# Kernel optimization log

Measured on AMD Instinct MI355X. Metric: run time of the kernel, lower is better.

## Reference

```python
import jax, jax.numpy as jnp
import numpy as np

KEEP_RATIO = 0.25
BLOCK = 8
TEMP = 0.1


def setup_inputs() -> dict:
    key = jax.random.key(0)
    features = jax.random.normal(key, (8, 256, 132, 132), dtype=jnp.float32)
    return {"features": features, "enabled": 1}


def reference(features, enabled):
    B, C, H, W = features.shape
    if not enabled:
        return jnp.ones((B, C, H, W), dtype=features.dtype)
    # pad H, W up to multiples of BLOCK (zeros, like F.pad default)
    ph = (-H) % BLOCK
    pw = (-W) % BLOCK
    x = jnp.pad(jnp.abs(features), ((0, 0), (0, 0), (0, ph), (0, pw)))
    Hp, Wp = H + ph, W + pw
    nh, nw = Hp // BLOCK, Wp // BLOCK
    # avg_pool2d(kernel=stride=BLOCK) == block-mean via reshape
    pooled = x.reshape(B, C, nh, BLOCK, nw, BLOCK).mean(axis=(3, 5))  # [B,C,nh,nw]
    total = nh * nw
    scores = pooled.reshape(B, C, total)
    keep = max(1, min(total, int(round(total * KEEP_RATIO))))
    top_vals, top_idx = jax.lax.top_k(scores, keep)  # sorted descending, like torch.topk
    # hard mask: scatter ones at topk indices
    flat_idx = top_idx.reshape(B * C, keep)
    hard = (jnp.zeros((B * C, total), dtype=features.dtype)
            .at[jnp.arange(B * C)[:, None], flat_idx].set(1.0)
            .reshape(B, C, total))
    # training-mode straight-through soft blend
    thr = jax.lax.stop_gradient(top_vals[..., -1:])  # kth value as threshold
    soft = jax.nn.sigmoid((scores - thr) / TEMP)
    soft = soft * (keep / jnp.maximum(soft.sum(-1, keepdims=True), 1e-6))
    soft = jnp.clip(soft, 0.0, 1.0)
    mask = jax.lax.stop_gradient(hard) - jax.lax.stop_gradient(soft) + soft
    # upsample blocks back to pixels (repeat_interleave) and crop padding
    block_mask = mask.reshape(B, C, nh, nw)
    full = jnp.repeat(jnp.repeat(block_mask, BLOCK, axis=2), BLOCK, axis=3)
    return full[:, :, :H, :W]
```

## Files before the change

### kernel.cpp

```cpp
#include <hip/hip_runtime.h>


#define HH 132
#define WW 132
#define NB 17
#define TOTAL 289
#define KEEP 72
#define NTHREADS 256
#define NV ((HH * WW) / 4)

typedef float floatx4 __attribute__((ext_vector_type(4)));

__global__ __launch_bounds__(NTHREADS)
void gate_kernel(const float4* __restrict__ feats4,
                 const int* __restrict__ enabled_p,
                 float4* __restrict__ out4) {
    const int plane = blockIdx.x;
    const int t = threadIdx.x;
    const float4* __restrict__ fp = feats4 + (size_t)plane * NV;
    floatx4* __restrict__ op = (floatx4*)(out4 + (size_t)plane * NV);

    __shared__ __align__(16) double s_score[TOTAL + 1];
    __shared__ float s_hard[TOTAL];

    for (int i = t; i < TOTAL + 1; i += NTHREADS)
        s_score[i] = (i < TOTAL) ? 0.0 : -1.0e300;
    __syncthreads();

    for (int v = t; v < NV; v += NTHREADS) {
        const float4 x = fp[v];
        const double s = (double)fabsf(x.x) + (double)fabsf(x.y)
                       + (double)fabsf(x.z) + (double)fabsf(x.w);
        const int base = v * 4;
        const int row = base / WW;
        const int col = base - row * WW;
        atomicAdd(&s_score[(row >> 3) * NB + (col >> 3)], s);
    }
    __syncthreads();

    const int en = *enabled_p;
    const double2* __restrict__ sc2 = (const double2*)s_score;
    for (int i = t; i < TOTAL; i += NTHREADS) {
        const double si = s_score[i];
        int rank = 0;
        #pragma unroll 5
        for (int q = 0; q < (TOTAL + 1) / 2; ++q) {
            const double2 sj = sc2[q];
            const int j = q * 2;
            rank += (int)((sj.x > si) || ((sj.x == si) && (j < i)));
            rank += (int)((sj.y > si) || ((sj.y == si) && (j + 1 < i)));
        }
        s_hard[i] = (!en || rank < KEEP) ? 1.0f : 0.0f;
    }
    __syncthreads();

    for (int v = t; v < NV; v += NTHREADS) {
        const int base = v * 4;
        const int row = base / WW;
        const int col = base - row * WW;
        const float m = s_hard[(row >> 3) * NB + (col >> 3)];
        const floatx4 mv = {m, m, m, m};
        __builtin_nontemporal_store(mv, &op[v]);
    }
}

extern "C" void kernel_launch(void* const* d_in, const int* in_sizes, int n_in,
                              void* d_out, int out_size, void* d_ws, size_t ws_size,
                              hipStream_t stream) {
    const float4* feats = (const float4*)d_in[0];
    const int* enabled = (const int*)d_in[1];
    float4* out = (float4*)d_out;
    const int planes = 8 * 256;
    gate_kernel<<<planes, NTHREADS, 0, stream>>>(feats, enabled, out);
}
```

Before: 260.4 us.

## Compute block scores per-thread and rank using 32-bit key prefilter

Replaces the per-element shared-memory double atomicAdd pooling with one thread per 8x8 block that sums its rows directly from global memory, removing atomic contention. The rank step compares the upper 32 bits of each double score as unsigned keys, four at a time, and falls back to the exact double comparison only when keys tie. The trade-off is strided, less coalesced global reads in the pooling pass, with only 289 of 256 threads' worth of work per plane (some threads do two blocks).

```diff
diff --git a/kernel.cpp b/kernel.cpp
--- a/kernel.cpp
+++ b/kernel.cpp
@@ -5,6 +5,7 @@
 #define WW 132
 #define NB 17
 #define TOTAL 289
+#define NPAD 320
 #define KEEP 72
 #define NTHREADS 256
 #define NV ((HH * WW) / 4)
@@ -20,35 +21,62 @@
     const float4* __restrict__ fp = feats4 + (size_t)plane * NV;
     floatx4* __restrict__ op = (floatx4*)(out4 + (size_t)plane * NV);
 
-    __shared__ __align__(16) double s_score[TOTAL + 1];
+    __shared__ __align__(16) double   s_score[NPAD];
+    __shared__ __align__(16) unsigned s_key[NPAD];
     __shared__ float s_hard[TOTAL];
 
-    for (int i = t; i < TOTAL + 1; i += NTHREADS)
-        s_score[i] = (i < TOTAL) ? 0.0 : -1.0e300;
+    for (int b = t; b < TOTAL; b += NTHREADS) {
+        const int br = b / NB;
+        const int bc = b - br * NB;
+        const int nr = (br == NB - 1) ? 4 : 8;
+        const int hc = (bc == NB - 1) ? 1 : 2;
+        const float4* bp = fp + br * (8 * 33) + bc * 2;
+        double a0 = 0.0, a1 = 0.0;
+        #pragma unroll
+        for (int rr = 0; rr < 8; ++rr) {
+            if (rr < nr) {
+                const float4 x = bp[rr * 33];
+                a0 += (double)fabsf(x.x) + (double)fabsf(x.y)
+                    + (double)fabsf(x.z) + (double)fabsf(x.w);
+                if (hc == 2) {
+                    const float4 y = bp[rr * 33 + 1];
+                    a1 += (double)fabsf(y.x) + (double)fabsf(y.y)
+                        + (double)fabsf(y.z) + (double)fabsf(y.w);
+                }
+            }
+        }
+        s_score[b] = a0 + a1;
+    }
+    if (t < NPAD - TOTAL) s_score[TOTAL + t] = 0.0;
     __syncthreads();
 
-    for (int v = t; v < NV; v += NTHREADS) {
-        const float4 x = fp[v];
-        const double s = (double)fabsf(x.x) + (double)fabsf(x.y)
-                       + (double)fabsf(x.z) + (double)fabsf(x.w);
-        const int base = v * 4;
-        const int row = base / WW;
-        const int col = base - row * WW;
-        atomicAdd(&s_score[(row >> 3) * NB + (col >> 3)], s);
+    for (int i = t; i < NPAD; i += NTHREADS) {
+        s_key[i] = (unsigned)((unsigned long long)
+                       __double_as_longlong(s_score[i]) >> 32);
     }
     __syncthreads();
 
     const int en = *enabled_p;
-    const double2* __restrict__ sc2 = (const double2*)s_score;
+    const uint4* __restrict__ sk4 = (const uint4*)s_key;
     for (int i = t; i < TOTAL; i += NTHREADS) {
-        const double si = s_score[i];
-        int rank = 0;
-        #pragma unroll 5
-        for (int q = 0; q < (TOTAL + 1) / 2; ++q) {
-            const double2 sj = sc2[q];
-            const int j = q * 2;
-            rank += (int)((sj.x > si) || ((sj.x == si) && (j < i)));
-            rank += (int)((sj.y > si) || ((sj.y == si) && (j + 1 < i)));
+        const unsigned ki = s_key[i];
+        int r = 0, e = 0;
+        #pragma unroll 10
+        for (int q = 0; q < NPAD / 4; ++q) {
+            const uint4 k = sk4[q];
+            r += (int)(k.x > ki) + (int)(k.y > ki)
+               + (int)(k.z > ki) + (int)(k.w > ki);
+            e += (int)(k.x == ki) + (int)(k.y == ki)
+               + (int)(k.z == ki) + (int)(k.w == ki);
+        }
+        int rank = r;
+        if (e > 1) {
+            const double si = s_score[i];
+            rank = 0;
+            for (int j = 0; j < TOTAL; ++j) {
+                const double sj = s_score[j];
+                rank += (int)((sj > si) || ((sj == si) && (j < i)));
+            }
         }
         s_hard[i] = (!en || rank < KEEP) ? 1.0f : 0.0f;
     }
```

Measured after the change: 278.0 us. +6.8%, slower.

## Replace shared double atomics with staged float4 sums and integer-key ranking

Applied to the files above, without the earlier changes.

Each thread now writes the per-float4 absolute sum into a 17KB shared array. One thread per block then gathers its block's entries and sums them in double, which removes the contended double-precision shared atomics. Scores are turned into unsigned float bit patterns so the rank computation uses integer compares over uint4 loads instead of double2 loads. The larger shared footprint may lower occupancy. Rounding each score to float can change how ties resolve compared with the double scores.

```diff
diff --git a/kernel.cpp b/kernel.cpp
--- a/kernel.cpp
+++ b/kernel.cpp
@@ -5,56 +5,79 @@
 #define WW 132
 #define NB 17
 #define TOTAL 289
+#define NKPAD 292
 #define KEEP 72
-#define NTHREADS 256
-#define NV ((HH * WW) / 4)
+#define NTH 256
+#define NC4 33
+#define NV 4356
+#define PLANES 2048
 
 typedef float floatx4 __attribute__((ext_vector_type(4)));
 
-__global__ __launch_bounds__(NTHREADS)
+__global__ __launch_bounds__(NTH)
 void gate_kernel(const float4* __restrict__ feats4,
                  const int* __restrict__ enabled_p,
                  float4* __restrict__ out4) {
     const int plane = blockIdx.x;
     const int t = threadIdx.x;
     const float4* __restrict__ fp = feats4 + (size_t)plane * NV;
-    floatx4* __restrict__ op = (floatx4*)(out4 + (size_t)plane * NV);
 
-    __shared__ __align__(16) double s_score[TOTAL + 1];
+    __shared__ __align__(16) float    s_e[NV];
+    __shared__ __align__(16) unsigned s_key[NKPAD];
     __shared__ float s_hard[TOTAL];
 
-    for (int i = t; i < TOTAL + 1; i += NTHREADS)
-        s_score[i] = (i < TOTAL) ? 0.0 : -1.0e300;
-    __syncthreads();
-
-    for (int v = t; v < NV; v += NTHREADS) {
-        const float4 x = fp[v];
-        const double s = (double)fabsf(x.x) + (double)fabsf(x.y)
-                       + (double)fabsf(x.z) + (double)fabsf(x.w);
-        const int base = v * 4;
-        const int row = base / WW;
-        const int col = base - row * WW;
-        atomicAdd(&s_score[(row >> 3) * NB + (col >> 3)], s);
+    #pragma unroll
+    for (int k = 0; k < 18; ++k) {
+        const int v = t + k * NTH;
+        if (v < NV) {
+            const float4 x = fp[v];
+            s_e[v] = (fabsf(x.x) + fabsf(x.y)) + (fabsf(x.z) + fabsf(x.w));
+        }
     }
     __syncthreads();
 
+    for (int b = t; b < TOTAL; b += NTH) {
+        const int br = b / NB;
+        const int bc = b - br * NB;
+        const int nr = (br == NB - 1) ? 4 : 8;
+        const int base = (br * 8) * NC4 + 2 * bc;
+        double sum = 0.0;
+        if (bc < NB - 1) {
+            for (int rr = 0; rr < nr; ++rr)
+                sum += (double)s_e[base + rr * NC4]
+                     + (double)s_e[base + rr * NC4 + 1];
+        } else {
+            for (int rr = 0; rr < nr; ++rr)
+                sum += (double)s_e[base + rr * NC4];
+        }
+        s_key[b] = __float_as_uint((float)sum);
+    }
+    if (t < NKPAD - TOTAL) s_key[TOTAL + t] = 0u;
+    __syncthreads();
+
     const int en = *enabled_p;
-    const double2* __restrict__ sc2 = (const double2*)s_score;
-    for (int i = t; i < TOTAL; i += NTHREADS) {
-        const double si = s_score[i];
+    for (int i = t; i < TOTAL; i += NTH) {
+        const unsigned ki = s_key[i];
+        const int thr0 = (i + 3) >> 2;
+        const int thr1 = (i + 2) >> 2;
+        const int thr2 = (i + 1) >> 2;
+        const int thr3 =  i      >> 2;
+        const uint4* __restrict__ sk4 = (const uint4*)s_key;
         int rank = 0;
-        #pragma unroll 5
-        for (int q = 0; q < (TOTAL + 1) / 2; ++q) {
-            const double2 sj = sc2[q];
-            const int j = q * 2;
-            rank += (int)((sj.x > si) || ((sj.x == si) && (j < i)));
-            rank += (int)((sj.y > si) || ((sj.y == si) && (j + 1 < i)));
+        #pragma unroll 8
+        for (int q = 0; q < NKPAD / 4; ++q) {
+            const uint4 k = sk4[q];
+            rank += (int)((k.x > ki) || ((k.x == ki) && (q < thr0)));
+            rank += (int)((k.y > ki) || ((k.y == ki) && (q < thr1)));
+            rank += (int)((k.z > ki) || ((k.z == ki) && (q < thr2)));
+            rank += (int)((k.w > ki) || ((k.w == ki) && (q < thr3)));
         }
         s_hard[i] = (!en || rank < KEEP) ? 1.0f : 0.0f;
     }
     __syncthreads();
 
-    for (int v = t; v < NV; v += NTHREADS) {
+    floatx4* __restrict__ op = (floatx4*)(out4 + (size_t)plane * NV);
+    for (int v = t; v < NV; v += NTH) {
         const int base = v * 4;
         const int row = base / WW;
         const int col = base - row * WW;
@@ -70,6 +93,5 @@
     const float4* feats = (const float4*)d_in[0];
     const int* enabled = (const int*)d_in[1];
     float4* out = (float4*)d_out;
-    const int planes = 8 * 256;
-    gate_kernel<<<planes, NTHREADS, 0, stream>>>(feats, enabled, out);
+    gate_kernel<<<PLANES, NTH, 0, stream>>>(feats, enabled, out);
 }
```

Result: no change. 256.2 us (-1.6%).
